# Optimization experiments

Hardware: AMD Instinct MI355X
Metric: run time of the kernel (lower is better)

The kernel has to match this reference:

```python
import jax, jax.numpy as jnp
import numpy as np

M = 50000   # eval points
N = 1024    # gaussians
EPS = 1e-6


def setup_inputs() -> dict:
    key = jax.random.key(0)
    k1, k2, k3 = jax.random.split(key, 3)
    points = jax.random.uniform(k1, (M, 3), dtype=jnp.float32)          # normalized coords in [0,1)
    positions = jax.random.uniform(k2, (N, 3), dtype=jnp.float32)       # torch.rand init
    log_scales = jnp.full((N, 3), -3.0, dtype=jnp.float32)              # torch.full(..., -3.0)
    intensities = jax.random.uniform(k3, (N,), dtype=jnp.float32) * 0.5  # torch.rand * 0.5
    return {"points": points, "positions": positions,
            "log_scales": log_scales, "intensities": intensities}


def reference(points, positions, log_scales, intensities):
    # Faithful translation of FastGaussianModel._eval_gaussians
    scales = jnp.exp(log_scales)                      # [N,3]
    inv_var = 1.0 / (scales ** 2 + EPS)               # [N,3]
    diff = points[:, None, :] - positions[None, :, :] # [M,N,3]
    quad = jnp.einsum('mnd,nd->mn', diff * diff, inv_var)  # [M,N]
    gauss = jnp.exp(-0.5 * quad)                      # [M,N]
    values = gauss @ intensities                      # [M]
    return values
```

## Files before the change

kernel.cpp:

```cpp
#include <hip/hip_runtime.h>


typedef float v2f __attribute__((ext_vector_type(2)));

constexpr int BLOCK         = 64;
constexpr int PTS_PER_LANE  = 4;
constexpr int TILE_PTS      = 256;
constexpr int TOTAL_SLICES  = 32;
constexpr int RECF          = 16;
constexpr int MAXPPS        = 48;
constexpr float KLN  = -0.7213475204444817f;
constexpr float FEPS = 1e-6f;


template <int PAIRS>
__device__ __forceinline__ void sweep_fast(const v2f* __restrict__ cp, int pairs,
                                           const float* px, const float* py,
                                           const float* pz, const float* pp,
                                           v2f* acc) {
    const int n = PAIRS > 0 ? PAIRS : pairs;
    #pragma unroll 4
    for (int i = 0; i < n; ++i) {
        v2f A0 = cp[0], A1 = cp[1], A2 = cp[2], C = cp[3], W = cp[4];
        cp += 8;
        #pragma unroll
        for (int j = 0; j < PTS_PER_LANE; ++j) {
            v2f t = C + (v2f){pp[j], pp[j]};
            t = __builtin_elementwise_fma(A2, (v2f){pz[j], pz[j]}, t);
            t = __builtin_elementwise_fma(A1, (v2f){py[j], py[j]}, t);
            t = __builtin_elementwise_fma(A0, (v2f){px[j], px[j]}, t);
            v2f g;
            g.x = __builtin_amdgcn_exp2f(t.x);
            g.y = __builtin_amdgcn_exp2f(t.y);
            acc[j] = __builtin_elementwise_fma(g, W, acc[j]);
        }
    }
}

template <int PAIRS>
__device__ __forceinline__ void sweep_full(const v2f* __restrict__ cp, int pairs,
                                           const float* px, const float* py,
                                           const float* pz, v2f* acc) {
    const int n = PAIRS > 0 ? PAIRS : pairs;
    #pragma unroll 2
    for (int i = 0; i < n; ++i) {
        v2f A0 = cp[0], A1 = cp[1], A2 = cp[2], C = cp[3], W = cp[4];
        v2f B0 = cp[5], B1 = cp[6], B2 = cp[7];
        cp += 8;
        #pragma unroll
        for (int j = 0; j < PTS_PER_LANE; ++j) {
            v2f t = __builtin_elementwise_fma(B0, (v2f){px[j]*px[j], px[j]*px[j]}, C);
            t = __builtin_elementwise_fma(B1, (v2f){py[j]*py[j], py[j]*py[j]}, t);
            t = __builtin_elementwise_fma(B2, (v2f){pz[j]*pz[j], pz[j]*pz[j]}, t);
            t = __builtin_elementwise_fma(A2, (v2f){pz[j], pz[j]}, t);
            t = __builtin_elementwise_fma(A1, (v2f){py[j], py[j]}, t);
            t = __builtin_elementwise_fma(A0, (v2f){px[j], px[j]}, t);
            v2f g;
            g.x = __builtin_amdgcn_exp2f(t.x);
            g.y = __builtin_amdgcn_exp2f(t.y);
            acc[j] = __builtin_elementwise_fma(g, W, acc[j]);
        }
    }
}

template <int PAIRS>
__global__ __launch_bounds__(BLOCK) void fgm_sweep(
        const float* __restrict__ points,
        const float* __restrict__ positions,
        const float* __restrict__ log_scales,
        const float* __restrict__ intensities,
        float* __restrict__ part,
        int M, int Mpad, int N, int pairsPerSlice) {
    constexpr int CPAIRS = PAIRS > 0 ? PAIRS : MAXPPS;
    __shared__ __align__(16) float recs[CPAIRS * RECF];

    const int lane  = threadIdx.x;
    const int slice = blockIdx.y;
    const int PPS   = PAIRS > 0 ? PAIRS : pairsPerSlice;
    const int m0    = blockIdx.x * TILE_PTS + 4 * lane;

    const float r0 = KLN / (__expf(2.0f * log_scales[0]) + FEPS);
    const float r1 = KLN / (__expf(2.0f * log_scales[1]) + FEPS);
    const float r2 = KLN / (__expf(2.0f * log_scales[2]) + FEPS);

    float px[4], py[4], pz[4], pp[4];
    if (m0 + 4 <= M) {
        const float4* p4 = (const float4*)(points + 3 * (size_t)m0);
        float4 f0 = p4[0], f1 = p4[1], f2 = p4[2];
        px[0] = f0.x; py[0] = f0.y; pz[0] = f0.z;
        px[1] = f0.w; py[1] = f1.x; pz[1] = f1.y;
        px[2] = f1.z; py[2] = f1.w; pz[2] = f2.x;
        px[3] = f2.y; py[3] = f2.z; pz[3] = f2.w;
    } else {
        #pragma unroll
        for (int j = 0; j < 4; ++j) {
            int m = m0 + j;
            float x = 0.f, y = 0.f, z = 0.f;
            if (m < M) { x = points[3*m+0]; y = points[3*m+1]; z = points[3*m+2]; }
            px[j] = x; py[j] = y; pz[j] = z;
        }
    }
    v2f acc[4];
    #pragma unroll
    for (int j = 0; j < 4; ++j) {
        pp[j] = r0*px[j]*px[j] + r1*py[j]*py[j] + r2*pz[j]*pz[j];
        acc[j] = (v2f){0.f, 0.f};
    }

    const int sliceBase = slice * PPS;
    for (int base = 0; base < PPS; base += CPAIRS) {
        const int cnt = (PPS - base < CPAIRS) ? (PPS - base) : CPAIRS;

        bool ok = true;
        for (int p = lane; p < cnt; p += 64) {
            const int g = (sliceBase + base + p) * 2;
            float q[6] = {0,0,0,0,0,0}, l[6] = {0,0,0,0,0,0}, w[2] = {0,0};
            bool val[2] = {g < N, g + 1 < N};
            if (val[1]) {
                const v2f* q2 = (const v2f*)(positions  + 3 * (size_t)g);
                const v2f* l2 = (const v2f*)(log_scales + 3 * (size_t)g);
                v2f Q01 = q2[0], Q23 = q2[1], Q45 = q2[2];
                v2f L01 = l2[0], L23 = l2[1], L45 = l2[2];
                v2f W01 = *(const v2f*)(intensities + g);
                q[0]=Q01.x; q[1]=Q01.y; q[2]=Q23.x; q[3]=Q23.y; q[4]=Q45.x; q[5]=Q45.y;
                l[0]=L01.x; l[1]=L01.y; l[2]=L23.x; l[3]=L23.y; l[4]=L45.x; l[5]=L45.y;
                w[0]=W01.x; w[1]=W01.y;
            } else if (val[0]) {
                q[0]=positions[3*g+0]; q[1]=positions[3*g+1]; q[2]=positions[3*g+2];
                l[0]=log_scales[3*g+0]; l[1]=log_scales[3*g+1]; l[2]=log_scales[3*g+2];
                w[0]=intensities[g];
            }
            float va[2][8];
            #pragma unroll
            for (int h = 0; h < 2; ++h) {
                float a0=0.f,a1=0.f,a2=0.f,b0=0.f,b1=0.f,b2=0.f,c=0.f,wt=0.f;
                if (val[h]) {
                    b0 = KLN / (__expf(2.0f*l[3*h+0]) + FEPS);
                    b1 = KLN / (__expf(2.0f*l[3*h+1]) + FEPS);
                    b2 = KLN / (__expf(2.0f*l[3*h+2]) + FEPS);
                    a0 = -2.f*b0*q[3*h+0];  a1 = -2.f*b1*q[3*h+1];  a2 = -2.f*b2*q[3*h+2];
                    c  = b0*q[3*h+0]*q[3*h+0] + b1*q[3*h+1]*q[3*h+1]
                       + b2*q[3*h+2]*q[3*h+2];
                    wt = w[h];
                    if (b0 != r0 || b1 != r1 || b2 != r2) ok = false;
                }
                va[h][0]=a0; va[h][1]=a1; va[h][2]=a2; va[h][3]=c;
                va[h][4]=wt; va[h][5]=b0; va[h][6]=b1; va[h][7]=b2;
            }
            v2f* r = (v2f*)&recs[p * RECF];
            #pragma unroll
            for (int k = 0; k < 8; ++k) r[k] = (v2f){va[0][k], va[1][k]};
        }
        const bool fast = __all(ok);
        __syncthreads();

        const v2f* cp = (const v2f*)recs;
        if (fast) sweep_fast<PAIRS>(cp, cnt, px, py, pz, pp, acc);
        else      sweep_full<PAIRS>(cp, cnt, px, py, pz, acc);
        if (base + CPAIRS < PPS) __syncthreads();
    }

    float4 vout = make_float4(acc[0].x + acc[0].y, acc[1].x + acc[1].y,
                              acc[2].x + acc[2].y, acc[3].x + acc[3].y);
    *(float4*)(part + (size_t)slice * Mpad + m0) = vout;
}

__global__ __launch_bounds__(256) void fgm_reduce(const float* __restrict__ part,
                                                  float* __restrict__ out,
                                                  int M, int Mpad, int out_n) {
    int m = blockIdx.x * 256 + threadIdx.x;
    if (m >= out_n) return;
    float s = 0.f;
    if (m < M) {
        #pragma unroll
        for (int sl = 0; sl < TOTAL_SLICES; ++sl)
            s += part[(size_t)sl * Mpad + m];
    }
    out[m] = s;
}

extern "C" void kernel_launch(void* const* d_in, const int* in_sizes, int n_in,
                              void* d_out, int out_size, void* d_ws, size_t ws_size,
                              hipStream_t stream) {
    const float* points      = (const float*)d_in[0];
    const float* positions   = (const float*)d_in[1];
    const float* log_scales  = (const float*)d_in[2];
    const float* intensities = (const float*)d_in[3];
    int M = in_sizes[0] / 3;
    int N = in_sizes[3];

    int Npairs = (N + 1) / 2;
    int PPS    = (Npairs + TOTAL_SLICES - 1) / TOTAL_SLICES;
    int tiles  = (M + TILE_PTS - 1) / TILE_PTS;
    int Mpad   = tiles * TILE_PTS;

    float* part = (float*)d_ws;

    dim3 grid(tiles, TOTAL_SLICES);
    if (PPS == 16) {
        fgm_sweep<16><<<grid, BLOCK, 0, stream>>>(points, positions, log_scales,
                                                  intensities, part, M, Mpad, N, PPS);
    } else {
        fgm_sweep<0><<<grid, BLOCK, 0, stream>>>(points, positions, log_scales,
                                                 intensities, part, M, Mpad, N, PPS);
    }

    int rblocks = (out_size + 255) / 256;
    fgm_reduce<<<rblocks, 256, 0, stream>>>(part, (float*)d_out, M, Mpad, out_size);
}
```

Before: 74.43 us.

## Fuse slice reduction into sweep kernel using per-wave gaussian slices in shared memory

The separate reduce kernel and the global partial-sum buffer are removed. Each block now has 8 waves, each handling one eighth of the gaussians over a 128-point tile, and the per-wave partial sums are combined in shared memory before writing the output directly. This saves a kernel launch and the round trip of 32 partial sums per point through global memory. In exchange each lane handles 2 points instead of 4, so less point data is reused per gaussian record load, and the block now needs a block-wide barrier. The grid becomes 1D with about 391 blocks of 512 threads.

```diff
diff --git a/kernel.cpp b/kernel.cpp
--- a/kernel.cpp
+++ b/kernel.cpp
@@ -3,12 +3,12 @@
 
 typedef float v2f __attribute__((ext_vector_type(2)));
 
-constexpr int BLOCK         = 64;
-constexpr int PTS_PER_LANE  = 4;
-constexpr int TILE_PTS      = 256;
-constexpr int TOTAL_SLICES  = 32;
-constexpr int RECF          = 16;
-constexpr int MAXPPS        = 48;
+constexpr int WAVES        = 8;
+constexpr int BLOCK        = 64 * WAVES;
+constexpr int PTS_PER_LANE = 2;
+constexpr int TILE_PTS     = 128;
+constexpr int RECF         = 16;
+constexpr int MAXPPS       = 64;
 constexpr float KLN  = -0.7213475204444817f;
 constexpr float FEPS = 1e-6f;
 
@@ -64,50 +64,49 @@
 }
 
 template <int PAIRS>
-__global__ __launch_bounds__(BLOCK) void fgm_sweep(
+__global__ __launch_bounds__(BLOCK) void fgm_fused(
         const float* __restrict__ points,
         const float* __restrict__ positions,
         const float* __restrict__ log_scales,
         const float* __restrict__ intensities,
-        float* __restrict__ part,
-        int M, int Mpad, int N, int pairsPerSlice) {
+        float* __restrict__ out,
+        int M, int N, int pairsPerSlice, int out_n) {
     constexpr int CPAIRS = PAIRS > 0 ? PAIRS : MAXPPS;
-    __shared__ __align__(16) float recs[CPAIRS * RECF];
-
-    const int lane  = threadIdx.x;
-    const int slice = blockIdx.y;
-    const int PPS   = PAIRS > 0 ? PAIRS : pairsPerSlice;
-    const int m0    = blockIdx.x * TILE_PTS + 4 * lane;
+    __shared__ __align__(16) float recs[WAVES][CPAIRS * RECF];
+    __shared__ float red[WAVES][TILE_PTS];
+
+    const int lane = threadIdx.x & 63;
+    const int wave = __builtin_amdgcn_readfirstlane(threadIdx.x >> 6);
+    const int PPS  = PAIRS > 0 ? PAIRS : pairsPerSlice;
+    const int m0   = blockIdx.x * TILE_PTS + PTS_PER_LANE * lane;
 
     const float r0 = KLN / (__expf(2.0f * log_scales[0]) + FEPS);
     const float r1 = KLN / (__expf(2.0f * log_scales[1]) + FEPS);
     const float r2 = KLN / (__expf(2.0f * log_scales[2]) + FEPS);
 
-    float px[4], py[4], pz[4], pp[4];
-    if (m0 + 4 <= M) {
-        const float4* p4 = (const float4*)(points + 3 * (size_t)m0);
-        float4 f0 = p4[0], f1 = p4[1], f2 = p4[2];
-        px[0] = f0.x; py[0] = f0.y; pz[0] = f0.z;
-        px[1] = f0.w; py[1] = f1.x; pz[1] = f1.y;
-        px[2] = f1.z; py[2] = f1.w; pz[2] = f2.x;
-        px[3] = f2.y; py[3] = f2.z; pz[3] = f2.w;
+    float px[2], py[2], pz[2], pp[2];
+    if (m0 + 2 <= M) {
+        const v2f* p2 = (const v2f*)(points + 3 * (size_t)m0);
+        v2f f0 = p2[0], f1 = p2[1], f2 = p2[2];
+        px[0] = f0.x; py[0] = f0.y; pz[0] = f1.x;
+        px[1] = f1.y; py[1] = f2.x; pz[1] = f2.y;
     } else {
         #pragma unroll
-        for (int j = 0; j < 4; ++j) {
+        for (int j = 0; j < 2; ++j) {
             int m = m0 + j;
             float x = 0.f, y = 0.f, z = 0.f;
             if (m < M) { x = points[3*m+0]; y = points[3*m+1]; z = points[3*m+2]; }
             px[j] = x; py[j] = y; pz[j] = z;
         }
     }
-    v2f acc[4];
+    v2f acc[2];
     #pragma unroll
-    for (int j = 0; j < 4; ++j) {
+    for (int j = 0; j < 2; ++j) {
         pp[j] = r0*px[j]*px[j] + r1*py[j]*py[j] + r2*pz[j]*pz[j];
         acc[j] = (v2f){0.f, 0.f};
     }
 
-    const int sliceBase = slice * PPS;
+    const int sliceBase = wave * PPS;
     for (int base = 0; base < PPS; base += CPAIRS) {
         const int cnt = (PPS - base < CPAIRS) ? (PPS - base) : CPAIRS;
 
@@ -147,36 +146,35 @@
                 va[h][0]=a0; va[h][1]=a1; va[h][2]=a2; va[h][3]=c;
                 va[h][4]=wt; va[h][5]=b0; va[h][6]=b1; va[h][7]=b2;
             }
-            v2f* r = (v2f*)&recs[p * RECF];
+            v2f* r = (v2f*)&recs[wave][p * RECF];
             #pragma unroll
             for (int k = 0; k < 8; ++k) r[k] = (v2f){va[0][k], va[1][k]};
         }
         const bool fast = __all(ok);
         __syncthreads();
 
-        const v2f* cp = (const v2f*)recs;
+        const v2f* cp = (const v2f*)recs[wave];
         if (fast) sweep_fast<PAIRS>(cp, cnt, px, py, pz, pp, acc);
         else      sweep_full<PAIRS>(cp, cnt, px, py, pz, acc);
         if (base + CPAIRS < PPS) __syncthreads();
     }
 
-    float4 vout = make_float4(acc[0].x + acc[0].y, acc[1].x + acc[1].y,
-                              acc[2].x + acc[2].y, acc[3].x + acc[3].y);
-    *(float4*)(part + (size_t)slice * Mpad + m0) = vout;
-}
-
-__global__ __launch_bounds__(256) void fgm_reduce(const float* __restrict__ part,
-                                                  float* __restrict__ out,
-                                                  int M, int Mpad, int out_n) {
-    int m = blockIdx.x * 256 + threadIdx.x;
-    if (m >= out_n) return;
-    float s = 0.f;
-    if (m < M) {
-        #pragma unroll
-        for (int sl = 0; sl < TOTAL_SLICES; ++sl)
-            s += part[(size_t)sl * Mpad + m];
-    }
-    out[m] = s;
+    red[wave][2*lane+0] = acc[0].x + acc[0].y;
+    red[wave][2*lane+1] = acc[1].x + acc[1].y;
+    __syncthreads();
+
+    if (threadIdx.x < TILE_PTS) {
+        int p = threadIdx.x;
+        int m = blockIdx.x * TILE_PTS + p;
+        if (m < out_n) {
+            float s = 0.f;
+            if (m < M) {
+                #pragma unroll
+                for (int w2 = 0; w2 < WAVES; ++w2) s += red[w2][p];
+            }
+            out[m] = s;
+        }
+    }
 }
 
 extern "C" void kernel_launch(void* const* d_in, const int* in_sizes, int n_in,
@@ -190,21 +188,18 @@
     int N = in_sizes[3];
 
     int Npairs = (N + 1) / 2;
-    int PPS    = (Npairs + TOTAL_SLICES - 1) / TOTAL_SLICES;
-    int tiles  = (M + TILE_PTS - 1) / TILE_PTS;
-    int Mpad   = tiles * TILE_PTS;
-
-    float* part = (float*)d_ws;
-
-    dim3 grid(tiles, TOTAL_SLICES);
-    if (PPS == 16) {
-        fgm_sweep<16><<<grid, BLOCK, 0, stream>>>(points, positions, log_scales,
-                                                  intensities, part, M, Mpad, N, PPS);
+    int PPS    = (Npairs + WAVES - 1) / WAVES;
+    int cover  = (M > out_size) ? M : out_size;
+    int tiles  = (cover + TILE_PTS - 1) / TILE_PTS;
+
+    dim3 grid(tiles);
+    if (PPS == 64) {
+        fgm_fused<64><<<grid, BLOCK, 0, stream>>>(points, positions, log_scales,
+                                                  intensities, (float*)d_out,
+                                                  M, N, PPS, out_size);
     } else {
-        fgm_sweep<0><<<grid, BLOCK, 0, stream>>>(points, positions, log_scales,
-                                                 intensities, part, M, Mpad, N, PPS);
-    }
-
-    int rblocks = (out_size + 255) / 256;
-    fgm_reduce<<<rblocks, 256, 0, stream>>>(part, (float*)d_out, M, Mpad, out_size);
-}
+        fgm_fused<0><<<grid, BLOCK, 0, stream>>>(points, positions, log_scales,
+                                                 intensities, (float*)d_out,
+                                                 M, N, PPS, out_size);
+    }
+}
```

Measured after the change: 72.31 us. -2.8%, faster.
